# Optimization experiments

Measured on AMD Instinct MI355X. Metric: run time of the kernel, lower is better.

Reference implementation:

```python
import jax, jax.numpy as jnp
import numpy as np

D = 1024      # model_dimension
H = 16        # num_heads
HD = D // H   # head_dimension (shared K/V head dim)
B, S = 2, 2048


def setup_inputs() -> dict:
    key = jax.random.key(0)
    ks = jax.random.split(key, 11)
    s = 0.02
    return {
        "q": jax.random.normal(ks[0], (B, S, D), jnp.float32),
        "k": jax.random.normal(ks[1], (B, S, D), jnp.float32),
        "v": jax.random.normal(ks[2], (B, S, D), jnp.float32),
        "Wq": jax.random.normal(ks[3], (D, D), jnp.float32) * s,
        "bq": jnp.zeros((D,), jnp.float32),
        "Wk": jax.random.normal(ks[4], (D, HD), jnp.float32) * s,
        "bk": jnp.zeros((HD,), jnp.float32),
        "Wv": jax.random.normal(ks[5], (D, HD), jnp.float32) * s,
        "bv": jnp.zeros((HD,), jnp.float32),
        "Wo": jax.random.normal(ks[6], (D, D), jnp.float32) * s,
        "bo": jnp.zeros((D,), jnp.float32),
    }


def reference(q, k, v, Wq, bq, Wk, bk, Wv, bv, Wo, bo):
    Bsz, Sq, Dm = q.shape
    # Q projection + split into heads: (B, H, Sq, HD)
    qh = (q @ Wq + bq).reshape(Bsz, Sq, H, HD).transpose(0, 2, 1, 3)
    # Shared single K/V head: (B, Sk, HD)
    kh = k @ Wk + bk
    vh = v @ Wv + bv
    # Scores (B, H, Sq, Sk), scaled then clamped as in the original
    scores = jnp.einsum('bhqd,bkd->bhqk', qh, kh) / jnp.sqrt(jnp.float32(HD))
    scores = jnp.clip(scores, -1e6, 1e6)
    attn = jax.nn.softmax(scores, axis=-1)
    out = jnp.einsum('bhqk,bkd->bhqd', attn, vh)
    out = out.transpose(0, 2, 1, 3).reshape(Bsz, Sq, Dm)
    return out @ Wo + bo
```

## Files before the change

### kernel.cpp

```cpp
#include <hip/hip_runtime.h>
#include <cstdint>
#include <cstddef>

typedef unsigned short u16;
typedef uint32_t u32;
typedef __bf16 bf16x8 __attribute__((ext_vector_type(8)));
typedef float  f32x4  __attribute__((ext_vector_type(4)));
typedef u16    u16x4  __attribute__((ext_vector_type(4)));
typedef u32    u32x4  __attribute__((ext_vector_type(4)));

#define DEV static __device__ __forceinline__
#define MFMA16(a, b, c) __builtin_amdgcn_mfma_f32_16x16x32_bf16(a, b, c, 0, 0, 0)

DEV u16 f2bf(float x) {
  unsigned u = __float_as_uint(x);
  u += 0x7fffu + ((u >> 16) & 1u);
  return (u16)(u >> 16);
}

DEV u32 cvt_pk_bf16(float lo, float hi) {
  u32 r;
  asm("v_cvt_pk_bf16_f32 %0, %1, %2" : "=v"(r) : "v"(lo), "v"(hi));
  return r;
}

DEV void gload_lds16(const void* g, void* l) {
  __builtin_amdgcn_global_load_lds(
      (__attribute__((address_space(1))) void*)(void*)g,
      (__attribute__((address_space(3))) void*)l, 16, 0, 0);
}

__global__ void k_transpose2(const float* __restrict__ in0, u16* __restrict__ out0,
                             const float* __restrict__ in1, u16* __restrict__ out1,
                             int R, int C) {
  __shared__ float tile[32][33];
  const float* in = blockIdx.z ? in1 : in0;
  u16* out = blockIdx.z ? out1 : out0;
  int bx = blockIdx.x * 32, by = blockIdx.y * 32;
  int tx = threadIdx.x, ty = threadIdx.y;
#pragma unroll
  for (int j = 0; j < 4; ++j)
    tile[ty + j * 8][tx] = in[(size_t)(by + ty + j * 8) * C + bx + tx];
  __syncthreads();
#pragma unroll
  for (int j = 0; j < 4; ++j)
    out[(size_t)(bx + ty + j * 8) * R + by + tx] = f2bf(tile[tx][ty + j * 8]);
}

template <bool OUT_BF16, bool A_FP32>
__global__ __launch_bounds__(512) void k_gemm128(const void* __restrict__ Ap, const u16* __restrict__ Bt,
                                                 const float* __restrict__ bias, void* __restrict__ Cout,
                                                 int M, int N, int K, float scale) {
  __shared__ u16 As[2][128 * 32];
  __shared__ u16 Bs[2][128 * 32];
  const int tid = threadIdx.x, lane = tid & 63, wid = tid >> 6;
  const int s = blockIdx.x;
  const int xr = s & 7, t = s >> 3;
  const int bx = t & 7;
  const int by = (t >> 3) * 8 + xr;
  const int brow = by * 128, bcol = bx * 128;
  const int wr = (wid >> 2) * 64, wc = (wid & 3) * 32;

  const int e0 = wid * 512 + lane * 8;
  const u16* b0 = Bt + (size_t)(bcol + (e0 >> 5)) * K + (e0 & 31);
  const u16* a0bf = A_FP32 ? nullptr : (const u16*)Ap + (size_t)(brow + (e0 >> 5)) * K + (e0 & 31);
  const float* a0f = A_FP32 ? (const float*)Ap + (size_t)(brow + (tid >> 2)) * K + (tid & 3) * 8 : nullptr;

  f32x4 ra0, ra1;
  auto LOADA = [&](int k0) {
    ra0 = *(const f32x4*)(a0f + k0);
    ra1 = *(const f32x4*)(a0f + k0 + 4);
  };
  auto WRITEA = [&](int buf) {
    u32x4 w;
    w[0] = cvt_pk_bf16(ra0[0], ra0[1]);
    w[1] = cvt_pk_bf16(ra0[2], ra0[3]);
    w[2] = cvt_pk_bf16(ra1[0], ra1[1]);
    w[3] = cvt_pk_bf16(ra1[2], ra1[3]);
    *(u32x4*)&As[buf][tid * 8] = w;
  };

  f32x4 acc[4][2] = {};
  const int NK = K / 32;
  if constexpr (A_FP32) {
    LOADA(0);
    gload_lds16(b0, &Bs[0][wid * 512]);
    WRITEA(0);
    LOADA(32);
    asm volatile("s_waitcnt lgkmcnt(0)" ::: "memory");
  } else {
    gload_lds16(a0bf, &As[0][wid * 512]);
    gload_lds16(b0, &Bs[0][wid * 512]);
  }
#pragma unroll 1
  for (int ks = 0; ks < NK; ++ks) {
    if (ks + 1 < NK) {
      if constexpr (A_FP32) {
        gload_lds16(b0 + (ks + 1) * 32, &Bs[(ks + 1) & 1][wid * 512]);
        asm volatile("s_waitcnt vmcnt(3)\n\ts_barrier" ::: "memory");
      } else {
        gload_lds16(a0bf + (ks + 1) * 32, &As[(ks + 1) & 1][wid * 512]);
        gload_lds16(b0 + (ks + 1) * 32, &Bs[(ks + 1) & 1][wid * 512]);
        asm volatile("s_waitcnt vmcnt(2)\n\ts_barrier" ::: "memory");
      }
    } else {
      asm volatile("s_waitcnt vmcnt(0)\n\ts_barrier" ::: "memory");
    }
    __builtin_amdgcn_sched_barrier(0);

    const u16* Ab = &As[ks & 1][0];
    const u16* Bb = &Bs[ks & 1][0];
    const int lr = lane & 15, lk = (lane >> 4) * 8;
    bf16x8 af[4], bfr[2];
#pragma unroll
    for (int m = 0; m < 4; ++m) af[m] = *(const bf16x8*)&Ab[(wr + m * 16 + lr) * 32 + lk];
#pragma unroll
    for (int n = 0; n < 2; ++n) bfr[n] = *(const bf16x8*)&Bb[(wc + n * 16 + lr) * 32 + lk];
    __builtin_amdgcn_s_setprio(1);
#pragma unroll
    for (int m = 0; m < 4; ++m)
#pragma unroll
      for (int n = 0; n < 2; ++n) acc[m][n] = MFMA16(af[m], bfr[n], acc[m][n]);
    __builtin_amdgcn_s_setprio(0);

    if constexpr (A_FP32) {
      if (ks + 1 < NK) {
        WRITEA((ks + 1) & 1);
        if (ks + 2 < NK) LOADA((ks + 2) * 32);
      }
      asm volatile("s_waitcnt lgkmcnt(0)\n\ts_barrier" ::: "memory");
    } else {
      asm volatile("s_barrier" ::: "memory");
    }
  }

  const int lr = lane & 15, lg = lane >> 4;
#pragma unroll
  for (int m = 0; m < 4; ++m)
#pragma unroll
    for (int n = 0; n < 2; ++n) {
      const int col = bcol + wc + n * 16 + lr;
      const float bv = bias ? bias[col] : 0.f;
#pragma unroll
      for (int r = 0; r < 4; ++r) {
        const int row = brow + wr + m * 16 + lg * 4 + r;
        float val = (acc[m][n][r] + bv) * scale;
        if constexpr (OUT_BF16) ((u16*)Cout)[(size_t)row * N + col] = f2bf(val);
        else ((float*)Cout)[(size_t)row * N + col] = val;
      }
    }
}

__global__ __launch_bounds__(256) void k_gemm64(const float* __restrict__ A0, const float* __restrict__ A1,
                                                const u16* __restrict__ Bt0, const u16* __restrict__ Bt1,
                                                const float* __restrict__ bias0, const float* __restrict__ bias1,
                                                u16* __restrict__ C0, u16* __restrict__ C1, int K) {
  __shared__ u16 As[2][64 * 32];
  __shared__ u16 Bs[2][64 * 32];
  const int sel = blockIdx.y;
  const float* Af = sel ? A1 : A0;
  const u16* Bt = sel ? Bt1 : Bt0;
  const float* bias = sel ? bias1 : bias0;
  const int tid = threadIdx.x, lane = tid & 63, wid = tid >> 6;
  const int brow = blockIdx.x * 64;
  const int e0 = wid * 512 + lane * 8;
  const u16* b0 = Bt + (size_t)(e0 >> 5) * K + (e0 & 31);
  const float* a0f = Af + (size_t)(brow + (tid >> 2)) * K + (tid & 3) * 8;

  f32x4 ra0, ra1;
  auto LOADA = [&](int k0) {
    ra0 = *(const f32x4*)(a0f + k0);
    ra1 = *(const f32x4*)(a0f + k0 + 4);
  };
  auto WRITEA = [&](int buf) {
    u32x4 w;
    w[0] = cvt_pk_bf16(ra0[0], ra0[1]);
    w[1] = cvt_pk_bf16(ra0[2], ra0[3]);
    w[2] = cvt_pk_bf16(ra1[0], ra1[1]);
    w[3] = cvt_pk_bf16(ra1[2], ra1[3]);
    *(u32x4*)&As[buf][tid * 8] = w;
  };

  f32x4 acc[4] = {};
  const int NK = K / 32;
  LOADA(0);
  gload_lds16(b0, &Bs[0][wid * 512]);
  WRITEA(0);
  LOADA(32);
  asm volatile("s_waitcnt lgkmcnt(0)" ::: "memory");
#pragma unroll 1
  for (int ks = 0; ks < NK; ++ks) {
    if (ks + 1 < NK) {
      gload_lds16(b0 + (ks + 1) * 32, &Bs[(ks + 1) & 1][wid * 512]);
      asm volatile("s_waitcnt vmcnt(3)\n\ts_barrier" ::: "memory");
    } else {
      asm volatile("s_waitcnt vmcnt(0)\n\ts_barrier" ::: "memory");
    }
    __builtin_amdgcn_sched_barrier(0);

    const u16* Ab = &As[ks & 1][0];
    const u16* Bb = &Bs[ks & 1][0];
    const int lr = lane & 15, lk = (lane >> 4) * 8;
    bf16x8 af = *(const bf16x8*)&Ab[(wid * 16 + lr) * 32 + lk];
    __builtin_amdgcn_s_setprio(1);
#pragma unroll
    for (int n = 0; n < 4; ++n) {
      bf16x8 bfr = *(const bf16x8*)&Bb[(n * 16 + lr) * 32 + lk];
      acc[n] = MFMA16(af, bfr, acc[n]);
    }
    __builtin_amdgcn_s_setprio(0);

    if (ks + 1 < NK) {
      WRITEA((ks + 1) & 1);
      if (ks + 2 < NK) LOADA((ks + 2) * 32);
    }
    asm volatile("s_waitcnt lgkmcnt(0)\n\ts_barrier" ::: "memory");
  }

  const int lr = lane & 15, lg = lane >> 4;
#pragma unroll
  for (int n = 0; n < 4; ++n) {
    const int col = n * 16 + lr;
    const float bv = bias[col];
#pragma unroll
    for (int r = 0; r < 4; ++r) {
      const int row = brow + wid * 16 + lg * 4 + r;
      const float val = acc[n][r] + bv;
      if (sel)
        C1[((size_t)(row >> 11) * 64 + col) * 2048 + (row & 2047)] = f2bf(val);
      else
        C0[(size_t)row * 64 + col] = f2bf(val);
    }
  }
}

__global__ __launch_bounds__(512) void k_attn(const u16* __restrict__ Qh, const u16* __restrict__ Kh,
                                              const u16* __restrict__ VhT, u16* __restrict__ Out) {
  constexpr int S = 2048, D = 1024, NT = 32;
  __shared__ u16 Ks[2][64 * 64];
  __shared__ u16 Vs[2][64 * 64];
  __shared__ u16 Ps[8][16 * 64];
  const int lane = threadIdx.x & 63, wid = threadIdx.x >> 6;
  const int lr = lane & 15, lg = lane >> 4;
  const int q0 = blockIdx.x * 128;
  const int h = blockIdx.y, b = blockIdx.z;

  bf16x8 qf[2];
#pragma unroll
  for (int kk = 0; kk < 2; ++kk)
    qf[kk] = *(const bf16x8*)&Qh[(size_t)(b * S + q0 + wid * 16 + lr) * D + h * 64 + kk * 32 + lg * 8];

  const int r8 = lane >> 3, ssl = (lane & 7) ^ r8;
  const u16* ksrc = Kh + (size_t)(b * S + wid * 8 + r8) * 64 + ssl * 8;
  const u16* vsrc = VhT + (size_t)(b * 64 + wid * 8 + r8) * S + ssl * 8;

  float lsum = 0.f;
  f32x4 o[4] = {};
  u16* Pw = &Ps[wid][0];
  const int pswz = (lr & 7) << 3;

  auto STAGE = [&](int buf, int t) {
    gload_lds16(ksrc + (size_t)(t * 64) * 64, &Ks[buf][(wid * 8) * 64]);
    gload_lds16(vsrc + t * 64, &Vs[buf][(wid * 8) * 64]);
  };

  STAGE(0, 0);
#pragma unroll 1
  for (int t = 0; t < NT; ++t) {
    if (t + 1 < NT) {
      STAGE((t + 1) & 1, t + 1);
      asm volatile("s_waitcnt vmcnt(2)\n\ts_barrier" ::: "memory");
    } else {
      asm volatile("s_waitcnt vmcnt(0)\n\ts_barrier" ::: "memory");
    }
    __builtin_amdgcn_sched_barrier(0);

    const u16* Kb = &Ks[t & 1][0];
    const u16* Vb = &Vs[t & 1][0];

    f32x4 z[4] = {};
    __builtin_amdgcn_s_setprio(1);
#pragma unroll
    for (int kk = 0; kk < 2; ++kk)
#pragma unroll
      for (int ct = 0; ct < 4; ++ct) {
        const int row = ct * 16 + lr;
        bf16x8 kf = *(const bf16x8*)&Kb[row * 64 + (((kk * 4 + lg) ^ (row & 7)) << 3)];
        z[ct] = MFMA16(kf, qf[kk], z[ct]);
      }
    __builtin_amdgcn_s_setprio(0);

    float s = 0.f;
#pragma unroll
    for (int ct = 0; ct < 4; ++ct) {
      const float p0 = __builtin_amdgcn_exp2f(z[ct][0]);
      const float p1 = __builtin_amdgcn_exp2f(z[ct][1]);
      const float p2 = __builtin_amdgcn_exp2f(z[ct][2]);
      const float p3 = __builtin_amdgcn_exp2f(z[ct][3]);
      s += (p0 + p1) + (p2 + p3);
      uint2 pk;
      pk.x = cvt_pk_bf16(p0, p1);
      pk.y = cvt_pk_bf16(p2, p3);
      *(uint2*)&Pw[lr * 64 + ((ct * 16 + lg * 4) ^ pswz)] = pk;
    }
    lsum += s;

#pragma unroll
    for (int kk = 0; kk < 2; ++kk) {
      bf16x8 pa = *(const bf16x8*)&Pw[lr * 64 + ((kk * 32 + lg * 8) ^ pswz)];
      __builtin_amdgcn_s_setprio(1);
#pragma unroll
      for (int nt = 0; nt < 4; ++nt) {
        const int row = nt * 16 + lr;
        bf16x8 vf = *(const bf16x8*)&Vb[row * 64 + (((kk * 4 + lg) ^ (row & 7)) << 3)];
        o[nt] = MFMA16(pa, vf, o[nt]);
      }
      __builtin_amdgcn_s_setprio(0);
    }
    asm volatile("s_barrier" ::: "memory");
  }

  lsum += __shfl_xor(lsum, 16);
  lsum += __shfl_xor(lsum, 32);
  const float linv = 1.f / lsum;
#pragma unroll
  for (int r = 0; r < 4; ++r) {
    const float li = __shfl(linv, (lane & 48) | (lg * 4 + r));
    const size_t row = (size_t)(b * S + q0 + wid * 16 + lg * 4 + r);
#pragma unroll
    for (int nt = 0; nt < 4; ++nt)
      Out[row * D + h * 64 + nt * 16 + lr] = f2bf(o[nt][r] * li);
  }
}

extern "C" void kernel_launch(void* const* d_in, const int* in_sizes, int n_in,
                              void* d_out, int out_size, void* d_ws, size_t ws_size,
                              hipStream_t stream) {
  const float* q  = (const float*)d_in[0];
  const float* k  = (const float*)d_in[1];
  const float* v  = (const float*)d_in[2];
  const float* Wq = (const float*)d_in[3];
  const float* bq = (const float*)d_in[4];
  const float* Wk = (const float*)d_in[5];
  const float* bk = (const float*)d_in[6];
  const float* Wv = (const float*)d_in[7];
  const float* bv = (const float*)d_in[8];
  const float* Wo = (const float*)d_in[9];
  const float* bo = (const float*)d_in[10];
  float* out = (float*)d_out;

  constexpr int B = 2, S = 2048, D = 1024, H = 16, HDc = 64;
  constexpr int M = B * S;

  char* ws = (char*)d_ws;
  size_t off = 0;
  auto alloc = [&](size_t bytes) { char* p = ws + off; off += bytes; return p; };
  u16* WqT  = (u16*)alloc((size_t)D * D * 2);
  u16* WkvT = (u16*)alloc((size_t)2 * HDc * D * 2);
  u16* WoT  = (u16*)alloc((size_t)D * D * 2);
  u16* Qh   = (u16*)alloc((size_t)M * D * 2);
  u16* Kh   = (u16*)alloc((size_t)M * HDc * 2);
  u16* VhT  = (u16*)alloc((size_t)M * HDc * 2);
  u16* AO   = (u16*)alloc((size_t)M * D * 2);
  u16* WkT = WkvT;
  u16* WvT = WkvT + (size_t)HDc * D;

  k_transpose2<<<dim3(D / 32, D / 32, 2), dim3(32, 8), 0, stream>>>(Wq, WqT, Wo, WoT, D, D);
  k_transpose2<<<dim3(HDc / 32, D / 32, 2), dim3(32, 8), 0, stream>>>(Wk, WkT, Wv, WvT, D, HDc);
  k_gemm128<true, true><<<dim3((M / 128) * (D / 128)), 512, 0, stream>>>(q, WqT, bq, Qh, M, D, D,
                                                                         0.125f * 1.44269504089f);
  k_gemm64<<<dim3(M / 64, 2), 256, 0, stream>>>(k, v, WkT, WvT, bk, bv, Kh, VhT, D);
  k_attn<<<dim3(S / 128, H, B), 512, 0, stream>>>(Qh, Kh, VhT, AO);
  k_gemm128<false, false><<<dim3((M / 128) * (D / 128)), 512, 0, stream>>>(AO, WoT, bo, out, M, D, D, 1.0f);
}
```

Baseline: 120.6 us.

## Fuse Q projection into attention kernel and merge weight transposes into one launch

The attention kernel now computes its own 128x64 Q tile per head by running a bf16 MFMA GEMM over the fp32 q input and the transposed Wq, then keeps the scaled result in LDS instead of reading a materialized Qh buffer. This removes the separate Q-projection GEMM launch and the 8 MB Qh write and re-read. The four weight transposes are merged into a single launch. In exchange each attention block reads its fp32 q rows from global memory once per head (16x redundant across heads). The Q GEMM inside the block uses a small 64-wide N tile, which may be less efficient than the dedicated GEMM.

```diff
diff --git a/kernel.cpp b/kernel.cpp
--- a/kernel.cpp
+++ b/kernel.cpp
@@ -30,12 +30,17 @@
       (__attribute__((address_space(3))) void*)l, 16, 0, 0);
 }
 
-__global__ void k_transpose2(const float* __restrict__ in0, u16* __restrict__ out0,
-                             const float* __restrict__ in1, u16* __restrict__ out1,
-                             int R, int C) {
+__global__ void k_transpose4(const float* __restrict__ Wq, u16* __restrict__ WqT,
+                             const float* __restrict__ Wo, u16* __restrict__ WoT,
+                             const float* __restrict__ Wk, u16* __restrict__ WkT,
+                             const float* __restrict__ Wv, u16* __restrict__ WvT) {
   __shared__ float tile[32][33];
-  const float* in = blockIdx.z ? in1 : in0;
-  u16* out = blockIdx.z ? out1 : out0;
+  const int z = blockIdx.z;
+  const int C = z < 2 ? 1024 : 64;
+  constexpr int R = 1024;
+  if (blockIdx.x * 32 >= C) return;
+  const float* in = z == 0 ? Wq : z == 1 ? Wo : z == 2 ? Wk : Wv;
+  u16* out = z == 0 ? WqT : z == 1 ? WoT : z == 2 ? WkT : WvT;
   int bx = blockIdx.x * 32, by = blockIdx.y * 32;
   int tx = threadIdx.x, ty = threadIdx.y;
 #pragma unroll
@@ -234,21 +239,93 @@
   }
 }
 
-__global__ __launch_bounds__(512) void k_attn(const u16* __restrict__ Qh, const u16* __restrict__ Kh,
-                                              const u16* __restrict__ VhT, u16* __restrict__ Out) {
-  constexpr int S = 2048, D = 1024, NT = 32;
-  __shared__ u16 Ks[2][64 * 64];
-  __shared__ u16 Vs[2][64 * 64];
-  __shared__ u16 Ps[8][16 * 64];
-  const int lane = threadIdx.x & 63, wid = threadIdx.x >> 6;
+__global__ __launch_bounds__(512) void k_attn(const float* __restrict__ qsrc, const u16* __restrict__ WqT,
+                                              const float* __restrict__ bq,
+                                              const u16* __restrict__ Kh, const u16* __restrict__ VhT,
+                                              u16* __restrict__ Out) {
+  constexpr int S = 2048, D = 1024, NT = 32, K = 1024;
+  __shared__ __align__(16) char smem[49152];
+  const int tid = threadIdx.x, lane = tid & 63, wid = tid >> 6;
   const int lr = lane & 15, lg = lane >> 4;
   const int q0 = blockIdx.x * 128;
   const int h = blockIdx.y, b = blockIdx.z;
 
+  u16* AsQ = (u16*)smem;
+  u16* BsQ = (u16*)(smem + 16384);
+  u16* Qlds = (u16*)(smem + 32768);
+
+  const float* a0f = qsrc + (size_t)(b * S + q0 + (tid >> 2)) * K + (tid & 3) * 8;
+  const int eB = (wid & 3) * 512 + lane * 8;
+  const u16* b0q = WqT + (size_t)(h * 64 + (eB >> 5)) * K + (eB & 31);
+
+  f32x4 ra0, ra1;
+  auto LOADA = [&](int k0) {
+    ra0 = *(const f32x4*)(a0f + k0);
+    ra1 = *(const f32x4*)(a0f + k0 + 4);
+  };
+  auto WRITEA = [&](int buf) {
+    u32x4 w;
+    w[0] = cvt_pk_bf16(ra0[0], ra0[1]);
+    w[1] = cvt_pk_bf16(ra0[2], ra0[3]);
+    w[2] = cvt_pk_bf16(ra1[0], ra1[1]);
+    w[3] = cvt_pk_bf16(ra1[2], ra1[3]);
+    *(u32x4*)&AsQ[buf * (128 * 32) + tid * 8] = w;
+  };
+
+  {
+    f32x4 accq[4] = {};
+    LOADA(0);
+    gload_lds16(b0q, &BsQ[(wid & 3) * 512]);
+    WRITEA(0);
+    LOADA(32);
+    asm volatile("s_waitcnt lgkmcnt(0)" ::: "memory");
+#pragma unroll 1
+    for (int ks = 0; ks < 32; ++ks) {
+      if (ks + 1 < 32) {
+        gload_lds16(b0q + (ks + 1) * 32, &BsQ[((ks + 1) & 1) * (64 * 32) + (wid & 3) * 512]);
+        asm volatile("s_waitcnt vmcnt(3)\n\ts_barrier" ::: "memory");
+      } else {
+        asm volatile("s_waitcnt vmcnt(0)\n\ts_barrier" ::: "memory");
+      }
+      __builtin_amdgcn_sched_barrier(0);
+
+      const u16* Ab = &AsQ[(ks & 1) * (128 * 32)];
+      const u16* Bb = &BsQ[(ks & 1) * (64 * 32)];
+      const int lk = (lane >> 4) * 8;
+      bf16x8 af = *(const bf16x8*)&Ab[(wid * 16 + lr) * 32 + lk];
+      __builtin_amdgcn_s_setprio(1);
+#pragma unroll
+      for (int n = 0; n < 4; ++n) {
+        bf16x8 bfr = *(const bf16x8*)&Bb[(n * 16 + lr) * 32 + lk];
+        accq[n] = MFMA16(af, bfr, accq[n]);
+      }
+      __builtin_amdgcn_s_setprio(0);
+
+      if (ks + 1 < 32) {
+        WRITEA((ks + 1) & 1);
+        if (ks + 2 < 32) LOADA((ks + 2) * 32);
+      }
+      asm volatile("s_waitcnt lgkmcnt(0)\n\ts_barrier" ::: "memory");
+    }
+    const float qscale = 0.125f * 1.44269504089f;
+#pragma unroll
+    for (int n = 0; n < 4; ++n) {
+      const float bv = bq[h * 64 + n * 16 + lr];
+#pragma unroll
+      for (int r = 0; r < 4; ++r)
+        Qlds[(wid * 16 + lg * 4 + r) * 64 + n * 16 + lr] = f2bf((accq[n][r] + bv) * qscale);
+    }
+    asm volatile("s_waitcnt vmcnt(0) lgkmcnt(0)\n\ts_barrier" ::: "memory");
+  }
+
+  u16* Ks0 = (u16*)smem;
+  u16* Vs0 = (u16*)(smem + 16384);
+  u16* Pw = Qlds + wid * (16 * 64);
+
   bf16x8 qf[2];
 #pragma unroll
   for (int kk = 0; kk < 2; ++kk)
-    qf[kk] = *(const bf16x8*)&Qh[(size_t)(b * S + q0 + wid * 16 + lr) * D + h * 64 + kk * 32 + lg * 8];
+    qf[kk] = *(const bf16x8*)&Qlds[(wid * 16 + lr) * 64 + kk * 32 + lg * 8];
 
   const int r8 = lane >> 3, ssl = (lane & 7) ^ r8;
   const u16* ksrc = Kh + (size_t)(b * S + wid * 8 + r8) * 64 + ssl * 8;
@@ -256,12 +333,11 @@
 
   float lsum = 0.f;
   f32x4 o[4] = {};
-  u16* Pw = &Ps[wid][0];
   const int pswz = (lr & 7) << 3;
 
   auto STAGE = [&](int buf, int t) {
-    gload_lds16(ksrc + (size_t)(t * 64) * 64, &Ks[buf][(wid * 8) * 64]);
-    gload_lds16(vsrc + t * 64, &Vs[buf][(wid * 8) * 64]);
+    gload_lds16(ksrc + (size_t)(t * 64) * 64, &Ks0[buf * (64 * 64) + (wid * 8) * 64]);
+    gload_lds16(vsrc + t * 64, &Vs0[buf * (64 * 64) + (wid * 8) * 64]);
   };
 
   STAGE(0, 0);
@@ -275,8 +351,8 @@
     }
     __builtin_amdgcn_sched_barrier(0);
 
-    const u16* Kb = &Ks[t & 1][0];
-    const u16* Vb = &Vs[t & 1][0];
+    const u16* Kb = &Ks0[(t & 1) * (64 * 64)];
+    const u16* Vb = &Vs0[(t & 1) * (64 * 64)];
 
     f32x4 z[4] = {};
     __builtin_amdgcn_s_setprio(1);
@@ -358,18 +434,14 @@
   u16* WqT  = (u16*)alloc((size_t)D * D * 2);
   u16* WkvT = (u16*)alloc((size_t)2 * HDc * D * 2);
   u16* WoT  = (u16*)alloc((size_t)D * D * 2);
-  u16* Qh   = (u16*)alloc((size_t)M * D * 2);
   u16* Kh   = (u16*)alloc((size_t)M * HDc * 2);
   u16* VhT  = (u16*)alloc((size_t)M * HDc * 2);
   u16* AO   = (u16*)alloc((size_t)M * D * 2);
   u16* WkT = WkvT;
   u16* WvT = WkvT + (size_t)HDc * D;
 
-  k_transpose2<<<dim3(D / 32, D / 32, 2), dim3(32, 8), 0, stream>>>(Wq, WqT, Wo, WoT, D, D);
-  k_transpose2<<<dim3(HDc / 32, D / 32, 2), dim3(32, 8), 0, stream>>>(Wk, WkT, Wv, WvT, D, HDc);
-  k_gemm128<true, true><<<dim3((M / 128) * (D / 128)), 512, 0, stream>>>(q, WqT, bq, Qh, M, D, D,
-                                                                         0.125f * 1.44269504089f);
+  k_transpose4<<<dim3(32, 32, 4), dim3(32, 8), 0, stream>>>(Wq, WqT, Wo, WoT, Wk, WkT, Wv, WvT);
   k_gemm64<<<dim3(M / 64, 2), 256, 0, stream>>>(k, v, WkT, WvT, bk, bv, Kh, VhT, D);
-  k_attn<<<dim3(S / 128, H, B), 512, 0, stream>>>(Qh, Kh, VhT, AO);
+  k_attn<<<dim3(S / 128, H, B), 512, 0, stream>>>(q, WqT, bq, Kh, VhT, AO);
   k_gemm128<false, false><<<dim3((M / 128) * (D / 128)), 512, 0, stream>>>(AO, WoT, bo, out, M, D, D, 1.0f);
 }
```

Measured after the change: 114.5 us. 1.05x faster.
